# Kernel optimization log

Hardware: AMD Instinct MI355X
Metric: run time of the kernel (lower is better)

Reference implementation:

```python
import jax, jax.numpy as jnp
import numpy as np
from jax import lax

B, H, W, C = 8, 128, 128, 256
NH, WS, SS = 8, 8, 4          # heads, window_size, shift_size
HD = C // NH                   # head_dim = 32
CK = 15                        # pe depthwise conv kernel (CK, 1)
HID = 4 * C                    # mlp hidden
N = WS * WS                    # tokens per window = 64
NW = (H // WS) * (W // WS)     # windows per image = 256
SCALE = HD ** -0.5


def _rel_index():
    coords = np.stack(np.meshgrid(np.arange(WS), np.arange(WS), indexing='ij'))  # (2,WS,WS)
    cf = coords.reshape(2, -1)
    rel = (cf[:, :, None] - cf[:, None, :]).transpose(1, 2, 0).astype(np.int64)
    rel[:, :, 0] += WS - 1
    rel[:, :, 1] += WS - 1
    rel[:, :, 0] *= 2 * WS - 1
    return rel.sum(-1)  # (N, N)

REL_IDX = jnp.asarray(_rel_index())


def _attn_mask():
    img = np.zeros((H, W), np.float32)
    cnt = 0
    for hs in (slice(0, -WS), slice(-WS, -SS), slice(-SS, None)):
        for ws_ in (slice(0, -WS), slice(-WS, -SS), slice(-SS, None)):
            img[hs, ws_] = cnt
            cnt += 1
    w = img.reshape(H // WS, WS, W // WS, WS).transpose(0, 2, 1, 3).reshape(NW, N)
    diff = w[:, None, :] - w[:, :, None]
    return jnp.asarray(np.where(diff != 0, -100.0, 0.0).astype(np.float32))  # (NW,N,N)

ATTN_MASK = _attn_mask()


def _window_partition(x):  # (B,H,W,C) -> (B*NW, N, C)
    x = x.reshape(B, H // WS, WS, W // WS, WS, C)
    return x.transpose(0, 1, 3, 2, 4, 5).reshape(-1, N, C)


def _window_reverse(w):  # (B*NW, N, C) -> (B,H,W,C)
    x = w.reshape(B, H // WS, W // WS, WS, WS, C)
    return x.transpose(0, 1, 3, 2, 4, 5).reshape(B, H, W, C)


def _ln(x, g, b):
    mu = jnp.mean(x, -1, keepdims=True)
    var = jnp.mean(jnp.square(x - mu), -1, keepdims=True)
    return (x - mu) * lax.rsqrt(var + 1e-5) * g + b


def setup_inputs() -> dict:
    key = jax.random.key(0)
    ks = jax.random.split(key, 8)
    def n(k, shape, s=0.02):
        return jax.random.normal(k, shape, jnp.float32) * s
    return {
        'x': jax.random.normal(ks[0], (B, H * W, C), jnp.float32),
        'norm1_g': jnp.ones((C,), jnp.float32), 'norm1_b': jnp.zeros((C,), jnp.float32),
        'qkv_w': n(ks[1], (3 * C, C)), 'qkv_b': jnp.zeros((3 * C,), jnp.float32),
        'rpb_table': n(ks[2], ((2 * WS - 1) ** 2, NH)),
        'pe_w': n(ks[3], (NH, 1, CK, 1)), 'pe_b': jnp.zeros((NH,), jnp.float32),
        'proj_w': n(ks[4], (C, C)), 'proj_b': jnp.zeros((C,), jnp.float32),
        'norm2_g': jnp.ones((C,), jnp.float32), 'norm2_b': jnp.zeros((C,), jnp.float32),
        'fc1_w': n(ks[5], (HID, C)), 'fc1_b': jnp.zeros((HID,), jnp.float32),
        'fc2_w': n(ks[6], (C, HID)), 'fc2_b': jnp.zeros((C,), jnp.float32),
    }


def reference(x, norm1_g, norm1_b, qkv_w, qkv_b, rpb_table, pe_w, pe_b,
              proj_w, proj_b, norm2_g, norm2_b, fc1_w, fc1_b, fc2_w, fc2_b):
    shortcut = x
    h = _ln(x, norm1_g, norm1_b).reshape(B, H, W, C)
    h = jnp.roll(h, (-SS, -SS), axis=(1, 2))            # cyclic shift
    win = _window_partition(h)                           # (B*NW, N, C)

    qkv = win @ qkv_w.T + qkv_b                          # (B*NW, N, 3C)
    qkv = qkv.reshape(-1, N, 3, NH, HD).transpose(2, 0, 3, 1, 4)
    q, k, v = qkv[0] * SCALE, qkv[1], qkv[2]             # (B*NW, NH, N, HD)
    attn = jnp.einsum('bhnd,bhmd->bhnm', q, k)           # (B*NW, NH, N, N)

    # learned conv positional term on attention logits (depthwise, kernel (CK,1))
    pe = lax.conv_general_dilated(
        attn, pe_w, window_strides=(1, 1), padding=[(CK // 2, CK // 2), (0, 0)],
        dimension_numbers=('NCHW', 'OIHW', 'NCHW'), feature_group_count=NH)
    attn = attn + pe + pe_b[None, :, None, None]

    # relative position bias
    rpb = rpb_table[REL_IDX.reshape(-1)].reshape(N, N, NH).transpose(2, 0, 1)
    attn = attn + rpb[None]

    # shift mask, softmax
    attn = attn.reshape(B, NW, NH, N, N) + ATTN_MASK[None, :, None]
    attn = jax.nn.softmax(attn.reshape(-1, NH, N, N), axis=-1)

    out = jnp.einsum('bhnm,bhmd->bhnd', attn, v)         # (B*NW, NH, N, HD)
    out = out.transpose(0, 2, 1, 3).reshape(-1, N, C)
    out = out @ proj_w.T + proj_b

    h = _window_reverse(out)                             # (B,H,W,C)
    h = jnp.roll(h, (SS, SS), axis=(1, 2)).reshape(B, H * W, C)
    x = shortcut + h

    y = _ln(x, norm2_g, norm2_b)
    y = jax.nn.gelu(y @ fc1_w.T + fc1_b, approximate=False)
    y = y @ fc2_w.T + fc2_b
    return x + y
```

## Files before the change

### kernel.cpp

```cpp
#include <hip/hip_runtime.h>


typedef unsigned short u16;
typedef unsigned int   u32;
typedef __attribute__((ext_vector_type(4))) int   ivec4;
typedef __attribute__((ext_vector_type(4))) float fvec4;
typedef __attribute__((ext_vector_type(8))) short svec8;
typedef __attribute__((ext_vector_type(4))) unsigned short usvec4;
typedef __attribute__((ext_vector_type(4))) float floatx4;

#define SCALE_Q 0.17677669529663687f

__device__ __forceinline__ u16 f2bf(float f) {
  union { float f; u32 u; } v; v.f = f;
  u32 r = v.u + 0x7FFFu + ((v.u >> 16) & 1u);
  return (u16)(r >> 16);
}
__device__ __forceinline__ float bf2f(u16 h) {
  union { u32 u; float f; } v; v.u = ((u32)h) << 16; return v.f;
}

__device__ __forceinline__ void async_copy16(const u16* g, u16* l) {
  __builtin_amdgcn_global_load_lds(
      (const __attribute__((address_space(1))) u32*)g,
      (__attribute__((address_space(3))) u32*)l, 16, 0, 0);
}

template<int SHIFT>
__global__ __launch_bounds__(256)
void ln_kernel(const float* __restrict__ x, const float* __restrict__ g,
               const float* __restrict__ b, u16* __restrict__ out)
{
  const int t    = blockIdx.x * 4 + (threadIdx.x >> 6);
  const int lane = threadIdx.x & 63;
  const int c    = lane * 4;
  size_t src;
  if constexpr (SHIFT) {
    int w  = t >> 6, tk = t & 63;
    int bi = w >> 8, wi = w & 255;
    int hr = ((wi >> 4) << 3) + (tk >> 3);
    int wr = ((wi & 15) << 3) + (tk & 7);
    int ho = (hr + 4) & 127, wo = (wr + 4) & 127;
    src = ((size_t)bi * 16384 + (size_t)ho * 128 + wo) * 256 + c;
  } else {
    src = (size_t)t * 256 + c;
  }
  fvec4 v = *(const fvec4*)(x + src);
  float s  = v.x + v.y + v.z + v.w;
  float s2 = v.x * v.x + v.y * v.y + v.z * v.z + v.w * v.w;
  #pragma unroll
  for (int o = 32; o > 0; o >>= 1) { s += __shfl_xor(s, o); s2 += __shfl_xor(s2, o); }
  float mu  = s * (1.0f / 256.0f);
  float var = s2 * (1.0f / 256.0f) - mu * mu;
  float inv = rsqrtf(var + 1e-5f);
  fvec4 gg = *(const fvec4*)(g + c);
  fvec4 bb = *(const fvec4*)(b + c);
  usvec4 o4;
  o4[0] = f2bf((v.x - mu) * inv * gg.x + bb.x);
  o4[1] = f2bf((v.y - mu) * inv * gg.y + bb.y);
  o4[2] = f2bf((v.z - mu) * inv * gg.z + bb.z);
  o4[3] = f2bf((v.w - mu) * inv * gg.w + bb.w);
  *(usvec4*)(out + (size_t)t * 256 + c) = o4;
}

__global__ __launch_bounds__(256)
void resid_ln2(const float* __restrict__ x, const u16* __restrict__ projout,
               const float* __restrict__ g, const float* __restrict__ b,
               float* __restrict__ x2, u16* __restrict__ yb)
{
  const int P    = blockIdx.x * 4 + (threadIdx.x >> 6);
  const int lane = threadIdx.x & 63;
  const int c    = lane * 4;
  const int bi = P >> 14, ho = (P >> 7) & 127, wo = P & 127;
  const int hr = (ho + 124) & 127, wr = (wo + 124) & 127;
  const int token = (((bi << 8) + ((hr >> 3) << 4) + (wr >> 3)) << 6)
                    + ((hr & 7) << 3) + (wr & 7);
  fvec4 xv = *(const fvec4*)(x + (size_t)P * 256 + c);
  usvec4 pv = *(const usvec4*)(projout + (size_t)token * 256 + c);
  fvec4 v;
  v.x = xv.x + bf2f(pv[0]); v.y = xv.y + bf2f(pv[1]);
  v.z = xv.z + bf2f(pv[2]); v.w = xv.w + bf2f(pv[3]);
  *(fvec4*)(x2 + (size_t)P * 256 + c) = v;
  float s  = v.x + v.y + v.z + v.w;
  float s2 = v.x * v.x + v.y * v.y + v.z * v.z + v.w * v.w;
  #pragma unroll
  for (int o = 32; o > 0; o >>= 1) { s += __shfl_xor(s, o); s2 += __shfl_xor(s2, o); }
  float mu  = s * (1.0f / 256.0f);
  float var = s2 * (1.0f / 256.0f) - mu * mu;
  float inv = rsqrtf(var + 1e-5f);
  fvec4 gg = *(const fvec4*)(g + c);
  fvec4 bb = *(const fvec4*)(b + c);
  usvec4 o4;
  o4[0] = f2bf((v.x - mu) * inv * gg.x + bb.x);
  o4[1] = f2bf((v.y - mu) * inv * gg.y + bb.y);
  o4[2] = f2bf((v.z - mu) * inv * gg.z + bb.z);
  o4[3] = f2bf((v.w - mu) * inv * gg.w + bb.w);
  *(usvec4*)(yb + (size_t)P * 256 + c) = o4;
}

__global__ __launch_bounds__(256)
void cvt_kernel(const float* __restrict__ src, u16* __restrict__ dst, int n) {
  int i = (blockIdx.x * 256 + threadIdx.x) * 4;
  if (i < n) {
    fvec4 v = *(const fvec4*)(src + i);
    usvec4 o; o[0] = f2bf(v.x); o[1] = f2bf(v.y); o[2] = f2bf(v.z); o[3] = f2bf(v.w);
    *(usvec4*)(dst + i) = o;
  }
}

__global__ __launch_bounds__(256)
void rpbm_kernel(const float* __restrict__ rpb, const float* __restrict__ pe_b,
                 float* __restrict__ out) {
  int idx = blockIdx.x * 256 + threadIdx.x;
  int m = idx & 63, n = (idx >> 6) & 63, hh = (idx >> 12) & 7, cls = idx >> 15;
  int dy = (n >> 3) - (m >> 3) + 7, dx = (n & 7) - (m & 7) + 7;
  float v = rpb[(dy * 15 + dx) * 8 + hh] + pe_b[hh];
  int lastR = cls >> 1, lastC = cls & 1;
  int rn = lastR ? (((n >> 3) < 4) ? 1 : 2) : 0;
  int cn = lastC ? (((n & 7) < 4) ? 1 : 2) : 0;
  int rm = lastR ? (((m >> 3) < 4) ? 1 : 2) : 0;
  int cm = lastC ? (((m & 7) < 4) ? 1 : 2) : 0;
  if (rn * 3 + cn != rm * 3 + cm) v -= 100.0f;
  out[idx] = v;
}

__global__ __launch_bounds__(256)
void mconv_kernel(const float* __restrict__ pe_w, u16* __restrict__ out) {
  int idx = blockIdx.x * 256 + threadIdx.x;
  int nn = idx & 63, n = (idx >> 6) & 63, hh = idx >> 12;
  int d = nn - n;
  float v = (d == 0) ? 1.0f : 0.0f;
  if (d >= -7 && d <= 7) v += pe_w[hh * 15 + d + 7];
  out[idx] = f2bf(v);
}

template<int EPI>
__global__ __launch_bounds__(512, 4)
void gemm4(const u16* __restrict__ A, const u16* __restrict__ Bw,
           const float* __restrict__ bias, u16* outb, float* outf,
           const float* __restrict__ extra, int N, int K, int row0)
{
  __shared__ __align__(16) u16 As[2][128 * 32];
  __shared__ __align__(16) u16 Bs[2][128 * 32];
  const int tid  = threadIdx.x;
  const int lane = tid & 63;
  const int wid  = tid >> 6;
  const int lo   = lane & 15, hi = lane >> 4;

  const int lin = blockIdx.y * gridDim.x + blockIdx.x;
  const int nwg = gridDim.x * gridDim.y;
  const int sw  = (lin & 7) * (nwg >> 3) + (lin >> 3);
  const int n0  = (sw % gridDim.x) * 128;
  const int m0  = (sw / gridDim.x) * 128;

  const int wm = (wid >> 1) * 32;
  const int wn = (wid & 1) * 64;

  floatx4 acc[2][4] = {};

  const int rr = tid >> 2, qq = tid & 3;

  auto issue = [&](int kt, int buf) {
    async_copy16(A  + (size_t)(m0 + rr) * K + kt + qq * 8, &As[buf][(size_t)tid * 8]);
    async_copy16(Bw + (size_t)(n0 + rr) * K + kt + qq * 8, &Bs[buf][(size_t)tid * 8]);
  };

  issue(0, 0);
  const int nk = K >> 5;
  for (int t = 0; t < nk; ++t) {
    __syncthreads();
    if (t + 1 < nk) issue((t + 1) << 5, (t + 1) & 1);
    const u16* as = As[t & 1];
    const u16* bs = Bs[t & 1];
    svec8 af[2], bfr[4];
    #pragma unroll
    for (int i = 0; i < 2; ++i)
      af[i] = *(const svec8*)&as[(wm + i * 16 + lo) * 32 + hi * 8];
    #pragma unroll
    for (int i = 0; i < 4; ++i)
      bfr[i] = *(const svec8*)&bs[(wn + i * 16 + lo) * 32 + hi * 8];
    #pragma unroll
    for (int mi = 0; mi < 2; ++mi)
      #pragma unroll
      for (int ni = 0; ni < 4; ++ni)
        acc[mi][ni] = __builtin_amdgcn_mfma_f32_16x16x32_bf16(af[mi], bfr[ni], acc[mi][ni], 0, 0, 0);
  }

  #pragma unroll
  for (int mi = 0; mi < 2; ++mi) {
    #pragma unroll
    for (int ni = 0; ni < 4; ++ni) {
      #pragma unroll
      for (int j = 0; j < 4; ++j) {
        int r = m0 + wm + mi * 16 + hi * 4 + j;
        int c = n0 + wn + ni * 16 + lo;
        float v = acc[mi][ni][j] + bias[c];
        if constexpr (EPI == 0) {
          if (c < 256) v *= SCALE_Q;
          outb[(size_t)r * N + c] = f2bf(v);
        } else if constexpr (EPI == 1) {
          outb[(size_t)r * N + c] = f2bf(v);
        } else if constexpr (EPI == 2) {
          float gv = 0.5f * v * (1.0f + erff(v * 0.70710678118654752f));
          outb[(size_t)r * N + c] = f2bf(gv);
        } else {
          size_t o = (size_t)(row0 + r) * N + c;
          outf[o] = extra[o] + v;
        }
      }
    }
  }
}

__global__ __launch_bounds__(256)
void attn2(const u16* __restrict__ qkv, const float* __restrict__ rpbm,
           const u16* __restrict__ mconv, u16* __restrict__ outb)
{
  __shared__ __align__(16) u16 Ks[64 * 40];
  __shared__ __align__(16) u16 Vt[32 * 72];
  __shared__ __align__(16) u16 ST[64 * 72];
  __shared__ __align__(16) u16 Pm[64 * 72];

  const int tid  = threadIdx.x;
  const int lane = tid & 63, wv = tid >> 6;
  const int lo   = lane & 15, hi = lane >> 4;
  const int wId  = blockIdx.x >> 3;
  const int h    = blockIdx.x & 7;
  const int wi   = wId & 255;
  const int cls  = (((wi >> 4) == 15) ? 2 : 0) + (((wi & 15) == 15) ? 1 : 0);
  const int m0   = wv * 16;

  {
    int r = tid >> 2, ch = tid & 3;
    const size_t base = (size_t)(wId * 64 + r) * 768 + h * 32 + ch * 8;
    *(ivec4*)&Ks[r * 40 + ch * 8] = *(const ivec4*)(qkv + base + 256);
    ivec4 vv = *(const ivec4*)(qkv + base + 512);
    const u16* pv = (const u16*)&vv;
    #pragma unroll
    for (int e = 0; e < 8; ++e) Vt[(ch * 8 + e) * 72 + r] = pv[e];
  }
  __syncthreads();

  {
    svec8 qa = *(const svec8*)(qkv + (size_t)(wId * 64 + m0 + lo) * 768 + h * 32 + hi * 8);
    floatx4 z = {0.f, 0.f, 0.f, 0.f};
    #pragma unroll
    for (int nb = 0; nb < 4; ++nb) {
      svec8 kb = *(const svec8*)&Ks[(nb * 16 + lo) * 40 + hi * 8];
      floatx4 s = __builtin_amdgcn_mfma_f32_16x16x32_bf16(qa, kb, z, 0, 0, 0);
      #pragma unroll
      for (int jp = 0; jp < 2; ++jp) {
        u32 pk = (u32)f2bf(s[jp * 2]) | ((u32)f2bf(s[jp * 2 + 1]) << 16);
        *(u32*)&ST[(nb * 16 + lo) * 72 + m0 + hi * 4 + jp * 2] = pk;
      }
    }
  }
  __syncthreads();

  floatx4 acc[4];
  {
    const float* rb = rpbm + (size_t)(cls * 8 + h) * 4096;
    #pragma unroll
    for (int nb = 0; nb < 4; ++nb)
      #pragma unroll
      for (int j = 0; j < 4; ++j)
        acc[nb][j] = rb[(m0 + hi * 4 + j) * 64 + nb * 16 + lo];
    svec8 mf0 = *(const svec8*)(mconv + ((h * 64 + m0 + lo) * 64 + hi * 8));
    svec8 mf1 = *(const svec8*)(mconv + ((h * 64 + m0 + lo) * 64 + 32 + hi * 8));
    #pragma unroll
    for (int nb = 0; nb < 4; ++nb) {
      svec8 st0 = *(const svec8*)&ST[(nb * 16 + lo) * 72 + hi * 8];
      svec8 st1 = *(const svec8*)&ST[(nb * 16 + lo) * 72 + 32 + hi * 8];
      acc[nb] = __builtin_amdgcn_mfma_f32_16x16x32_bf16(mf0, st0, acc[nb], 0, 0, 0);
      acc[nb] = __builtin_amdgcn_mfma_f32_16x16x32_bf16(mf1, st1, acc[nb], 0, 0, 0);
    }
  }

  {
    float ev[4][4], inv[4];
    #pragma unroll
    for (int j = 0; j < 4; ++j) {
      float m_ = fmaxf(fmaxf(acc[0][j], acc[1][j]), fmaxf(acc[2][j], acc[3][j]));
      m_ = fmaxf(m_, __shfl_xor(m_, 1)); m_ = fmaxf(m_, __shfl_xor(m_, 2));
      m_ = fmaxf(m_, __shfl_xor(m_, 4)); m_ = fmaxf(m_, __shfl_xor(m_, 8));
      #pragma unroll
      for (int nb = 0; nb < 4; ++nb) ev[nb][j] = __expf(acc[nb][j] - m_);
      float s_ = ev[0][j] + ev[1][j] + ev[2][j] + ev[3][j];
      s_ += __shfl_xor(s_, 1); s_ += __shfl_xor(s_, 2);
      s_ += __shfl_xor(s_, 4); s_ += __shfl_xor(s_, 8);
      inv[j] = __builtin_amdgcn_rcpf(s_);
    }
    #pragma unroll
    for (int nb = 0; nb < 4; ++nb)
      #pragma unroll
      for (int j = 0; j < 4; ++j)
        Pm[(m0 + hi * 4 + j) * 72 + nb * 16 + lo] = f2bf(ev[nb][j] * inv[j]);
  }
  __syncthreads();

  {
    floatx4 oacc[2] = {};
    #pragma unroll
    for (int ks = 0; ks < 2; ++ks) {
      svec8 pa = *(const svec8*)&Pm[(m0 + lo) * 72 + ks * 32 + hi * 8];
      #pragma unroll
      for (int nb = 0; nb < 2; ++nb) {
        svec8 vb = *(const svec8*)&Vt[(nb * 16 + lo) * 72 + ks * 32 + hi * 8];
        oacc[nb] = __builtin_amdgcn_mfma_f32_16x16x32_bf16(pa, vb, oacc[nb], 0, 0, 0);
      }
    }
    #pragma unroll
    for (int nb = 0; nb < 2; ++nb)
      #pragma unroll
      for (int j = 0; j < 4; ++j)
        outb[(size_t)(wId * 64 + m0 + hi * 4 + j) * 256 + h * 32 + nb * 16 + lo] = f2bf(oacc[nb][j]);
  }
}

extern "C" void kernel_launch(void* const* d_in, const int* in_sizes, int n_in,
                              void* d_out, int out_size, void* d_ws, size_t ws_size,
                              hipStream_t stream)
{
  const float* x      = (const float*)d_in[0];
  const float* n1g    = (const float*)d_in[1];
  const float* n1b    = (const float*)d_in[2];
  const float* qkv_w  = (const float*)d_in[3];
  const float* qkv_b  = (const float*)d_in[4];
  const float* rpb    = (const float*)d_in[5];
  const float* pe_w   = (const float*)d_in[6];
  const float* pe_b   = (const float*)d_in[7];
  const float* proj_w = (const float*)d_in[8];
  const float* proj_b = (const float*)d_in[9];
  const float* n2g    = (const float*)d_in[10];
  const float* n2b    = (const float*)d_in[11];
  const float* fc1_w  = (const float*)d_in[12];
  const float* fc1_b  = (const float*)d_in[13];
  const float* fc2_w  = (const float*)d_in[14];
  const float* fc2_b  = (const float*)d_in[15];
  float* outf = (float*)d_out;

  char* ws = (char*)d_ws;
  u16* qkvb    = (u16*)ws;
  u16* winb    = (u16*)(ws + (192ull << 20));
  u16* yb      = (u16*)ws;
  u16* h1b     = (u16*)(ws + (64ull << 20));
  u16* projoutb= (u16*)(ws + (128ull << 20));
  u16* fc1wb   = (u16*)(ws + (192ull << 20));
  u16* fc2wb   = (u16*)(ws + (192ull << 20) + (1ull << 19));

  u16*   qkvwb  = (u16*)d_out;
  float* rpbmT  = (float*)((char*)d_out + (1ull << 19));
  u16*   mconvT = (u16*)((char*)d_out + (1ull << 20));
  u16*   projwb = (u16*)((char*)d_out + (1ull << 20) + (1ull << 18));

  cvt_kernel<<<192, 256, 0, stream>>>(qkv_w, qkvwb, 196608);
  rpbm_kernel<<<512, 256, 0, stream>>>(rpb, pe_b, rpbmT);
  mconv_kernel<<<128, 256, 0, stream>>>(pe_w, mconvT);
  cvt_kernel<<<64, 256, 0, stream>>>(proj_w, projwb, 65536);

  ln_kernel<1><<<32768, 256, 0, stream>>>(x, n1g, n1b, winb);
  gemm4<0><<<dim3(6, 1024), 512, 0, stream>>>(winb, qkvwb, qkv_b, qkvb, nullptr, nullptr, 768, 256, 0);
  attn2<<<16384, 256, 0, stream>>>(qkvb, rpbmT, mconvT, winb);
  gemm4<1><<<dim3(2, 1024), 512, 0, stream>>>(winb, projwb, proj_b, projoutb, nullptr, nullptr, 256, 256, 0);
  cvt_kernel<<<256, 256, 0, stream>>>(fc1_w, fc1wb, 262144);
  cvt_kernel<<<256, 256, 0, stream>>>(fc2_w, fc2wb, 262144);
  resid_ln2<<<32768, 256, 0, stream>>>(x, projoutb, n2g, n2b, outf, yb);
  for (int half = 0; half < 2; ++half) {
    int r0 = half * 65536;
    gemm4<2><<<dim3(8, 512), 512, 0, stream>>>(yb + (size_t)r0 * 256, fc1wb, fc1_b, h1b, nullptr, nullptr, 1024, 256, 0);
    gemm4<3><<<dim3(2, 512), 512, 0, stream>>>(h1b, fc2wb, fc2_b, nullptr, outf, outf, 256, 1024, r0);
  }
}
```

Measured before the change: 879.5 us.

## Replace double-buffered GEMM with weight-stationary LDS GEMM streaming A from global

Replaces the 128x128 double-buffered async-copy GEMM with a kernel that loads a full 128x256 weight slab into swizzled LDS once per block. Each wave then streams its A rows straight from global into registers across several M sub-tiles, so the weight tile is reused across 512 or 256 rows. The grid is remapped so consecutive blocks spread across XCDs. The aim is to cut repeated B-tile loads and per-K-step barriers. In exchange it uses 64KB of LDS per block, which limits occupancy, and A loads are no longer coalesced through LDS, with nothing overlapping them.

```diff
diff --git a/kernel.cpp b/kernel.cpp
--- a/kernel.cpp
+++ b/kernel.cpp
@@ -18,12 +18,6 @@
 }
 __device__ __forceinline__ float bf2f(u16 h) {
   union { u32 u; float f; } v; v.u = ((u32)h) << 16; return v.f;
-}
-
-__device__ __forceinline__ void async_copy16(const u16* g, u16* l) {
-  __builtin_amdgcn_global_load_lds(
-      (const __attribute__((address_space(1))) u32*)g,
-      (__attribute__((address_space(3))) u32*)l, 16, 0, 0);
 }
 
 template<int SHIFT>
@@ -134,81 +128,128 @@
   out[idx] = f2bf(v);
 }
 
-template<int EPI>
+template<int EPI, int KCHUNKS, int NSPB>
 __global__ __launch_bounds__(512, 4)
-void gemm4(const u16* __restrict__ A, const u16* __restrict__ Bw,
-           const float* __restrict__ bias, u16* outb, float* outf,
-           const float* __restrict__ extra, int N, int K, int row0)
+void sgemm(const u16* __restrict__ A, const u16* __restrict__ Bw,
+           const float* __restrict__ bias, u16* __restrict__ outb, float* outf,
+           const float* extra, int N, int row0, int gy)
 {
-  __shared__ __align__(16) u16 As[2][128 * 32];
-  __shared__ __align__(16) u16 Bs[2][128 * 32];
+  constexpr int K = KCHUNKS * 256;
+  __shared__ __align__(16) u16 Ws[128 * 256];
+
   const int tid  = threadIdx.x;
   const int lane = tid & 63;
-  const int wid  = tid >> 6;
+  const int wv   = tid >> 6;
   const int lo   = lane & 15, hi = lane >> 4;
 
-  const int lin = blockIdx.y * gridDim.x + blockIdx.x;
-  const int nwg = gridDim.x * gridDim.y;
-  const int sw  = (lin & 7) * (nwg >> 3) + (lin >> 3);
-  const int n0  = (sw % gridDim.x) * 128;
-  const int m0  = (sw / gridDim.x) * 128;
-
-  const int wm = (wid >> 1) * 32;
-  const int wn = (wid & 1) * 64;
-
-  floatx4 acc[2][4] = {};
-
-  const int rr = tid >> 2, qq = tid & 3;
-
-  auto issue = [&](int kt, int buf) {
-    async_copy16(A  + (size_t)(m0 + rr) * K + kt + qq * 8, &As[buf][(size_t)tid * 8]);
-    async_copy16(Bw + (size_t)(n0 + rr) * K + kt + qq * 8, &Bs[buf][(size_t)tid * 8]);
-  };
-
-  issue(0, 0);
-  const int nk = K >> 5;
-  for (int t = 0; t < nk; ++t) {
-    __syncthreads();
-    if (t + 1 < nk) issue((t + 1) << 5, (t + 1) & 1);
-    const u16* as = As[t & 1];
-    const u16* bs = Bs[t & 1];
-    svec8 af[2], bfr[4];
-    #pragma unroll
-    for (int i = 0; i < 2; ++i)
-      af[i] = *(const svec8*)&as[(wm + i * 16 + lo) * 32 + hi * 8];
-    #pragma unroll
-    for (int i = 0; i < 4; ++i)
-      bfr[i] = *(const svec8*)&bs[(wn + i * 16 + lo) * 32 + hi * 8];
-    #pragma unroll
-    for (int mi = 0; mi < 2; ++mi)
-      #pragma unroll
-      for (int ni = 0; ni < 4; ++ni)
-        acc[mi][ni] = __builtin_amdgcn_mfma_f32_16x16x32_bf16(af[mi], bfr[ni], acc[mi][ni], 0, 0, 0);
-  }
-
+  const int hb  = blockIdx.x;
+  const int xcd = hb & 7;
+  const int j   = hb >> 3;
+  const int ns  = j % gy;
+  const int mb  = (j / gy) * 8 + xcd;
+  const int n0  = ns * 128;
+  const size_t mbase = (size_t)mb * (128 * NSPB);
+
+  int bo[8];
   #pragma unroll
-  for (int mi = 0; mi < 2; ++mi) {
-    #pragma unroll
-    for (int ni = 0; ni < 4; ++ni) {
-      #pragma unroll
-      for (int j = 0; j < 4; ++j) {
-        int r = m0 + wm + mi * 16 + hi * 4 + j;
-        int c = n0 + wn + ni * 16 + lo;
-        float v = acc[mi][ni][j] + bias[c];
+  for (int kk = 0; kk < 8; ++kk) {
+    int u  = kk * 4 + hi;
+    int up = (u & 24) | ((u ^ lo) & 7);
+    bo[kk] = lo * 256 + up * 8;
+  }
+
+  const int wr = tid >> 2, wq = tid & 3;
+
+  auto epilogue = [&](floatx4 (&a)[8], size_t ms0) {
+    #pragma unroll
+    for (int nt = 0; nt < 8; ++nt) {
+      int c = n0 + nt * 16 + lo;
+      float bv = bias[c];
+      #pragma unroll
+      for (int jj = 0; jj < 4; ++jj) {
+        size_t r = ms0 + hi * 4 + jj;
+        float v = a[nt][jj] + bv;
         if constexpr (EPI == 0) {
           if (c < 256) v *= SCALE_Q;
-          outb[(size_t)r * N + c] = f2bf(v);
+          outb[r * N + c] = f2bf(v);
         } else if constexpr (EPI == 1) {
-          outb[(size_t)r * N + c] = f2bf(v);
+          outb[r * N + c] = f2bf(v);
         } else if constexpr (EPI == 2) {
           float gv = 0.5f * v * (1.0f + erff(v * 0.70710678118654752f));
-          outb[(size_t)r * N + c] = f2bf(gv);
+          outb[r * N + c] = f2bf(gv);
         } else {
           size_t o = (size_t)(row0 + r) * N + c;
           outf[o] = extra[o] + v;
         }
       }
     }
+  };
+
+  if constexpr (KCHUNKS == 1) {
+    {
+      const u16* src = Bw + (size_t)(n0 + wr) * K;
+      #pragma unroll
+      for (int i = 0; i < 8; ++i) {
+        int u  = wq * 8 + i;
+        int up = (u & 24) | ((u ^ wr) & 7);
+        *(ivec4*)&Ws[wr * 256 + up * 8] = *(const ivec4*)(src + u * 8);
+      }
+    }
+    __syncthreads();
+    #pragma unroll 1
+    for (int s = 0; s < NSPB; ++s) {
+      const size_t ms0 = mbase + s * 128 + wv * 16;
+      const u16* arow = A + (ms0 + lo) * (size_t)K;
+      svec8 af[8];
+      #pragma unroll
+      for (int kk = 0; kk < 8; ++kk)
+        af[kk] = *(const svec8*)(arow + kk * 32 + hi * 8);
+      floatx4 acc[8] = {};
+      #pragma unroll
+      for (int nt = 0; nt < 8; ++nt) {
+        #pragma unroll
+        for (int kk = 0; kk < 8; ++kk) {
+          svec8 bfr = *(const svec8*)&Ws[nt * 4096 + bo[kk]];
+          acc[nt] = __builtin_amdgcn_mfma_f32_16x16x32_bf16(af[kk], bfr, acc[nt], 0, 0, 0);
+        }
+      }
+      epilogue(acc, ms0);
+    }
+  } else {
+    floatx4 acc[NSPB][8] = {};
+    for (int c = 0; c < KCHUNKS; ++c) {
+      if (c) __syncthreads();
+      {
+        const u16* src = Bw + (size_t)(n0 + wr) * K + c * 256;
+        #pragma unroll
+        for (int i = 0; i < 8; ++i) {
+          int u  = wq * 8 + i;
+          int up = (u & 24) | ((u ^ wr) & 7);
+          *(ivec4*)&Ws[wr * 256 + up * 8] = *(const ivec4*)(src + u * 8);
+        }
+      }
+      __syncthreads();
+      #pragma unroll
+      for (int s = 0; s < NSPB; ++s) {
+        const size_t ms0 = mbase + s * 128 + wv * 16;
+        const u16* arow = A + (ms0 + lo) * (size_t)K + c * 256;
+        svec8 af[8];
+        #pragma unroll
+        for (int kk = 0; kk < 8; ++kk)
+          af[kk] = *(const svec8*)(arow + kk * 32 + hi * 8);
+        #pragma unroll
+        for (int nt = 0; nt < 8; ++nt) {
+          #pragma unroll
+          for (int kk = 0; kk < 8; ++kk) {
+            svec8 bfr = *(const svec8*)&Ws[nt * 4096 + bo[kk]];
+            acc[s][nt] = __builtin_amdgcn_mfma_f32_16x16x32_bf16(af[kk], bfr, acc[s][nt], 0, 0, 0);
+          }
+        }
+      }
+    }
+    #pragma unroll
+    for (int s = 0; s < NSPB; ++s)
+      epilogue(acc[s], mbase + s * 128 + wv * 16);
   }
 }
 
@@ -359,15 +400,15 @@
   cvt_kernel<<<64, 256, 0, stream>>>(proj_w, projwb, 65536);
 
   ln_kernel<1><<<32768, 256, 0, stream>>>(x, n1g, n1b, winb);
-  gemm4<0><<<dim3(6, 1024), 512, 0, stream>>>(winb, qkvwb, qkv_b, qkvb, nullptr, nullptr, 768, 256, 0);
+  sgemm<0, 1, 4><<<1536, 512, 0, stream>>>(winb, qkvwb, qkv_b, qkvb, nullptr, nullptr, 768, 0, 6);
   attn2<<<16384, 256, 0, stream>>>(qkvb, rpbmT, mconvT, winb);
-  gemm4<1><<<dim3(2, 1024), 512, 0, stream>>>(winb, projwb, proj_b, projoutb, nullptr, nullptr, 256, 256, 0);
+  sgemm<1, 1, 4><<<512, 512, 0, stream>>>(winb, projwb, proj_b, projoutb, nullptr, nullptr, 256, 0, 2);
   cvt_kernel<<<256, 256, 0, stream>>>(fc1_w, fc1wb, 262144);
   cvt_kernel<<<256, 256, 0, stream>>>(fc2_w, fc2wb, 262144);
   resid_ln2<<<32768, 256, 0, stream>>>(x, projoutb, n2g, n2b, outf, yb);
   for (int half = 0; half < 2; ++half) {
     int r0 = half * 65536;
-    gemm4<2><<<dim3(8, 512), 512, 0, stream>>>(yb + (size_t)r0 * 256, fc1wb, fc1_b, h1b, nullptr, nullptr, 1024, 256, 0);
-    gemm4<3><<<dim3(2, 512), 512, 0, stream>>>(h1b, fc2wb, fc2_b, nullptr, outf, outf, 256, 1024, r0);
-  }
-}
+    sgemm<2, 1, 4><<<1024, 512, 0, stream>>>(yb + (size_t)r0 * 256, fc1wb, fc1_b, h1b, nullptr, nullptr, 1024, 0, 8);
+    sgemm<3, 4, 2><<<512, 512, 0, stream>>>(h1b, fc2wb, fc2_b, nullptr, outf, outf, 256, r0, 2);
+  }
+}
```

Result: slower. 2.413 ms (+174.4%).

## Fuse fc1+GELU+fc2 MLP into one kernel keeping hidden activations on-chip

Applied to the files above, without the earlier changes.

Replaces the two-GEMM MLP (fc1 with GELU epilogue, then fc2 with residual add) with a single kernel in which each wave computes 16 rows. It chunks the hidden dimension, applies GELU, stages the chunk in LDS, and accumulates fc2 output in registers. This removes the round trip of the large hidden activation through global memory and a set of launches. In exchange, weights are read per wave directly from global memory with no LDS tiling or cross-wave reuse, so cache pressure and load latency rise.

```diff
diff --git a/kernel.cpp b/kernel.cpp
--- a/kernel.cpp
+++ b/kernel.cpp
@@ -198,16 +198,81 @@
         if constexpr (EPI == 0) {
           if (c < 256) v *= SCALE_Q;
           outb[(size_t)r * N + c] = f2bf(v);
-        } else if constexpr (EPI == 1) {
+        } else {
           outb[(size_t)r * N + c] = f2bf(v);
-        } else if constexpr (EPI == 2) {
-          float gv = 0.5f * v * (1.0f + erff(v * 0.70710678118654752f));
-          outb[(size_t)r * N + c] = f2bf(gv);
-        } else {
-          size_t o = (size_t)(row0 + r) * N + c;
-          outf[o] = extra[o] + v;
         }
       }
+    }
+  }
+}
+
+__global__ __launch_bounds__(512)
+void mlp_fused(const u16* __restrict__ yb, const u16* __restrict__ w1,
+               const float* __restrict__ b1, const u16* __restrict__ w2,
+               const float* __restrict__ b2, float* __restrict__ xio)
+{
+  __shared__ __align__(16) u16 hbuf[8][16 * 72];
+  const int tid  = threadIdx.x;
+  const int lane = tid & 63;
+  const int wv   = tid >> 6;
+  const int lo   = lane & 15, hi = lane >> 4;
+  const int r0   = blockIdx.x * 128 + wv * 16;
+
+  const u16* arow = yb + (size_t)(r0 + lo) * 256;
+  svec8 af[8];
+  #pragma unroll
+  for (int kk = 0; kk < 8; ++kk)
+    af[kk] = *(const svec8*)(arow + kk * 32 + hi * 8);
+
+  u16* myh = &hbuf[wv][0];
+  floatx4 oacc[16] = {};
+
+  #pragma unroll 1
+  for (int hc = 0; hc < 16; ++hc) {
+    const int h0 = hc * 64;
+    floatx4 facc[4];
+    #pragma unroll
+    for (int nb = 0; nb < 4; ++nb) {
+      float bv = b1[h0 + nb * 16 + lo];
+      facc[nb] = (floatx4){bv, bv, bv, bv};
+    }
+    #pragma unroll
+    for (int nb = 0; nb < 4; ++nb) {
+      const u16* wrow = w1 + (size_t)(h0 + nb * 16 + lo) * 256;
+      #pragma unroll
+      for (int kk = 0; kk < 8; ++kk) {
+        svec8 bfr = *(const svec8*)(wrow + kk * 32 + hi * 8);
+        facc[nb] = __builtin_amdgcn_mfma_f32_16x16x32_bf16(af[kk], bfr, facc[nb], 0, 0, 0);
+      }
+    }
+    #pragma unroll
+    for (int nb = 0; nb < 4; ++nb)
+      #pragma unroll
+      for (int j = 0; j < 4; ++j) {
+        float v  = facc[nb][j];
+        float gv = 0.5f * v * (1.0f + erff(v * 0.70710678118654752f));
+        myh[(hi * 4 + j) * 72 + nb * 16 + lo] = f2bf(gv);
+      }
+    #pragma unroll
+    for (int ks = 0; ks < 2; ++ks) {
+      svec8 pa = *(const svec8*)&myh[lo * 72 + ks * 32 + hi * 8];
+      #pragma unroll
+      for (int nt = 0; nt < 16; ++nt) {
+        const u16* w2p = w2 + (size_t)(nt * 16 + lo) * 1024 + h0 + ks * 32 + hi * 8;
+        svec8 bfr = *(const svec8*)w2p;
+        oacc[nt] = __builtin_amdgcn_mfma_f32_16x16x32_bf16(pa, bfr, oacc[nt], 0, 0, 0);
+      }
+    }
+  }
+
+  #pragma unroll
+  for (int nt = 0; nt < 16; ++nt) {
+    int c = nt * 16 + lo;
+    float bv = b2[c];
+    #pragma unroll
+    for (int j = 0; j < 4; ++j) {
+      size_t o = (size_t)(r0 + hi * 4 + j) * 256 + c;
+      xio[o] = xio[o] + oacc[nt][j] + bv;
     }
   }
 }
@@ -343,8 +408,7 @@
   u16* qkvb    = (u16*)ws;
   u16* winb    = (u16*)(ws + (192ull << 20));
   u16* yb      = (u16*)ws;
-  u16* h1b     = (u16*)(ws + (64ull << 20));
-  u16* projoutb= (u16*)(ws + (128ull << 20));
+  u16* projoutb= (u16*)(ws + (64ull << 20));
   u16* fc1wb   = (u16*)(ws + (192ull << 20));
   u16* fc2wb   = (u16*)(ws + (192ull << 20) + (1ull << 19));
 
@@ -365,9 +429,5 @@
   cvt_kernel<<<256, 256, 0, stream>>>(fc1_w, fc1wb, 262144);
   cvt_kernel<<<256, 256, 0, stream>>>(fc2_w, fc2wb, 262144);
   resid_ln2<<<32768, 256, 0, stream>>>(x, projoutb, n2g, n2b, outf, yb);
-  for (int half = 0; half < 2; ++half) {
-    int r0 = half * 65536;
-    gemm4<2><<<dim3(8, 512), 512, 0, stream>>>(yb + (size_t)r0 * 256, fc1wb, fc1_b, h1b, nullptr, nullptr, 1024, 256, 0);
-    gemm4<3><<<dim3(2, 512), 512, 0, stream>>>(h1b, fc2wb, fc2_b, nullptr, outf, outf, 256, 1024, r0);
-  }
-}
+  mlp_fused<<<1024, 512, 0, stream>>>(yb, fc1wb, fc1_b, fc2wb, fc2_b, outf);
+}
```

New measurement: 1.535 ms. 74.5% more time.
